# Kernel optimization log

Hardware: AMD Instinct MI355X
Metric: run time of the kernel (lower is better)

The kernel has to match this reference:

```python
import jax, jax.numpy as jnp
from jax import lax
import numpy as np

DECAY = 0.9
THRESH = 1.0


def setup_inputs() -> dict:
    key = jax.random.key(0)
    k1, k2, k3 = jax.random.split(key, 3)
    B, T, I, H, O = 64, 256, 1024, 2048, 1024
    x = jax.random.normal(k1, (B, T, I), dtype=jnp.float32)
    W1 = jax.random.normal(k2, (I, H), dtype=jnp.float32) * (1.0 / np.sqrt(I))
    b1 = jnp.zeros((H,), dtype=jnp.float32)
    W2 = jax.random.normal(k3, (H, O), dtype=jnp.float32) * (1.0 / np.sqrt(H))
    b2 = jnp.zeros((O,), dtype=jnp.float32)
    return {"x": x, "W1": W1, "b1": b1, "W2": W2, "b2": b2}


def reference(x, W1, b1, W2, b2):
    B, T, I = x.shape
    H = W1.shape[1]
    # Batch fc1 across all timesteps in one GEMM: [B,T,H]
    cur = jnp.einsum('bti,ih->bth', x, W1) + b1
    cur_tm = jnp.swapaxes(cur, 0, 1)  # [T,B,H] time-major for scan

    def step(carry, cur_t):
        mem, _ = carry
        mem = mem * DECAY + cur_t * (1.0 - DECAY)
        fired = mem > THRESH
        spk = jnp.where(fired, 1.0, 0.0).astype(mem.dtype)
        mem = jnp.where(fired, 0.0, mem)
        return (mem, spk), None

    mem0 = jnp.zeros((B, H), dtype=x.dtype)
    spk0 = jnp.zeros((B, H), dtype=x.dtype)
    (_, spk_last), _ = lax.scan(step, (mem0, spk0), cur_tm)
    # fc2 applied only to the final spike pattern, as in the original
    return spk_last @ W2 + b2
```

## Files before the change

kernel.cpp:

```cpp
#include <hip/hip_runtime.h>


typedef __attribute__((ext_vector_type(16))) float f32x16;
typedef __attribute__((ext_vector_type(8))) short s16x8;

#define GPTR(p) ((const __attribute__((address_space(1))) void*)(p))
#define SPTR(p) ((__attribute__((address_space(3))) void*)(p))

static constexpr int Bsz = 64, Tsz = 256, Isz = 1024, Hsz = 2048, Osz = 1024;
static constexpr int BK = 32;
static constexpr int NKT = Isz / BK;
static constexpr int AH_OFF = 0, AL_OFF = 8192, BH_OFF = 16384, BL_OFF = 24576;
static constexpr int BUFEL = 32768;
static constexpr int SCAN_STRIDE = 260;
static constexpr int LDS_USHORTS = 128 * SCAN_STRIDE * 2;

__device__ __forceinline__ unsigned short f2bf(float f) {
  unsigned u = __float_as_uint(f);
  u += 0x7FFFu + ((u >> 16) & 1u);
  return (unsigned short)(u >> 16);
}
__device__ __forceinline__ float bf2f(unsigned short h) {
  return __uint_as_float(((unsigned)h) << 16);
}

__global__ void split_x_kernel(const float* __restrict__ x,
                               unsigned short* __restrict__ hi,
                               unsigned short* __restrict__ lo) {
  const long i = (long)blockIdx.x * 256 + threadIdx.x;
  const float4 v = ((const float4*)x)[i];
  const unsigned short hx = f2bf(v.x), hy = f2bf(v.y), hz = f2bf(v.z), hw = f2bf(v.w);
  ushort4 H, L;
  H.x = hx; H.y = hy; H.z = hz; H.w = hw;
  L.x = f2bf(v.x - bf2f(hx));
  L.y = f2bf(v.y - bf2f(hy));
  L.z = f2bf(v.z - bf2f(hz));
  L.w = f2bf(v.w - bf2f(hw));
  ((ushort4*)hi)[i] = H;
  ((ushort4*)lo)[i] = L;
}

__global__ void w1_transpose_split_kernel(const float* __restrict__ W1,
                                          unsigned short* __restrict__ wh,
                                          unsigned short* __restrict__ wl) {
  __shared__ float tile[32][33];
  const int h0 = blockIdx.x * 32;
  const int i0 = blockIdx.y * 32;
  const int c = threadIdx.x & 31;
  const int r4 = threadIdx.x >> 5;
#pragma unroll
  for (int s = 0; s < 4; ++s) {
    const int r = r4 + s * 8;
    tile[r][c] = W1[(long)(i0 + r) * Hsz + h0 + c];
  }
  __syncthreads();
#pragma unroll
  for (int s = 0; s < 4; ++s) {
    const int hr = r4 + s * 8;
    const float v = tile[c][hr];
    const unsigned short hh = f2bf(v);
    wh[(long)(h0 + hr) * Isz + i0 + c] = hh;
    wl[(long)(h0 + hr) * Isz + i0 + c] = f2bf(v - bf2f(hh));
  }
}

__global__ __launch_bounds__(512, 2) void gemm1_scan_kernel(
    const unsigned short* __restrict__ xh, const unsigned short* __restrict__ xl,
    const unsigned short* __restrict__ wth, const unsigned short* __restrict__ wtl,
    const float* __restrict__ b1, float* __restrict__ spk) {
  __shared__ __align__(16) unsigned short lds[LDS_USHORTS];

  const int tid = threadIdx.x;
  const int l = tid & 63;
  const int w = tid >> 6;
  const int wm = w >> 2;
  const int wn = w & 3;
  const int b = blockIdx.y;
  const int hb = blockIdx.x * 256;

  const int srow = tid >> 2;
  const int gch8 = ((tid & 3) ^ ((tid >> 3) & 3)) * 8;
  const long aoff0 = (long)(b * Tsz + srow) * Isz + gch8;
  const long aoff1 = (long)(b * Tsz + 128 + srow) * Isz + gch8;
  const long boff0 = (long)(hb + srow) * Isz + gch8;
  const long boff1 = (long)(hb + 128 + srow) * Isz + gch8;
  const unsigned short* gAh0 = xh + aoff0;  const unsigned short* gAh1 = xh + aoff1;
  const unsigned short* gAl0 = xl + aoff0;  const unsigned short* gAl1 = xl + aoff1;
  const unsigned short* gBh0 = wth + boff0; const unsigned short* gBh1 = wth + boff1;
  const unsigned short* gBl0 = wtl + boff0; const unsigned short* gBl1 = wtl + boff1;

#define STG(OFF, G0, G1, KT) do {                                                      \
    unsigned short* d_ = lds + ((KT) & 1) * BUFEL + (OFF) + tid * 8;                   \
    __builtin_amdgcn_global_load_lds(GPTR((G0) + (long)(KT) * BK), SPTR(d_), 16, 0, 0);\
    __builtin_amdgcn_global_load_lds(GPTR((G1) + (long)(KT) * BK), SPTR(d_ + 4096), 16, 0, 0); \
  } while (0)

  const int lr = l & 31;
  const int swzf = (l >> 1) & 3;
  const int chK0 = (((l >> 5)) ^ swzf) * 8;
  const int chK1 = ((2 + (l >> 5)) ^ swzf) * 8;
  const int abase = (wm * 128 + lr) * 32;
  const int bbase = (wn * 64 + lr) * 32;

  f32x16 acc[4][2];
#pragma unroll
  for (int i = 0; i < 4; ++i)
#pragma unroll
    for (int j = 0; j < 2; ++j) acc[i][j] = (f32x16)(0.f);

#define MM(MI, NI, AF, BF) \
  acc[MI][NI] = __builtin_amdgcn_mfma_f32_32x32x16_bf16(AF, BF, acc[MI][NI], 0, 0, 0)

#define BAR() __builtin_amdgcn_s_barrier()
#define LGKM0() do { asm volatile("s_waitcnt lgkmcnt(0)" ::: "memory");                \
    __builtin_amdgcn_sched_barrier(0); } while (0)

  STG(AH_OFF, gAh0, gAh1, 0);
  STG(BH_OFF, gBh0, gBh1, 0);
  STG(AL_OFF, gAl0, gAl1, 0);
  STG(BL_OFF, gBl0, gBl1, 0);
  asm volatile("s_waitcnt vmcnt(0)" ::: "memory");
  BAR();

  s16x8 Ah0[4], Ah1[4], Al0[4], Al1[4], Bh0[2], Bh1[2], Bl0[2], Bl1[2];

  for (int kt = 0; kt < NKT; ++kt) {
    const unsigned short* p = lds + (kt & 1) * BUFEL;
    const bool st = (kt + 1) < NKT;

#pragma unroll
    for (int mi = 0; mi < 4; ++mi) {
      Ah0[mi] = *(const s16x8*)(p + AH_OFF + abase + mi * 1024 + chK0);
      Ah1[mi] = *(const s16x8*)(p + AH_OFF + abase + mi * 1024 + chK1);
    }
#pragma unroll
    for (int ni = 0; ni < 2; ++ni) {
      Bh0[ni] = *(const s16x8*)(p + BH_OFF + bbase + ni * 1024 + chK0);
      Bh1[ni] = *(const s16x8*)(p + BH_OFF + bbase + ni * 1024 + chK1);
    }
    if (st) { STG(AH_OFF, gAh0, gAh1, kt + 1); STG(BH_OFF, gBh0, gBh1, kt + 1); }
    BAR();
    LGKM0();
    __builtin_amdgcn_s_setprio(1);
    MM(0, 0, Ah0[0], Bh0[0]); MM(0, 1, Ah0[0], Bh0[1]);
    MM(1, 0, Ah0[1], Bh0[0]); MM(1, 1, Ah0[1], Bh0[1]);
    MM(2, 0, Ah0[2], Bh0[0]); MM(2, 1, Ah0[2], Bh0[1]);
    MM(3, 0, Ah0[3], Bh0[0]); MM(3, 1, Ah0[3], Bh0[1]);
    MM(0, 0, Ah1[0], Bh1[0]); MM(0, 1, Ah1[0], Bh1[1]);
    MM(1, 0, Ah1[1], Bh1[0]); MM(1, 1, Ah1[1], Bh1[1]);
    MM(2, 0, Ah1[2], Bh1[0]); MM(2, 1, Ah1[2], Bh1[1]);
    MM(3, 0, Ah1[3], Bh1[0]); MM(3, 1, Ah1[3], Bh1[1]);
    __builtin_amdgcn_s_setprio(0);
    if (st) asm volatile("s_waitcnt vmcnt(4)" ::: "memory");
    else    asm volatile("s_waitcnt vmcnt(0)" ::: "memory");
    BAR();

#pragma unroll
    for (int mi = 0; mi < 4; ++mi) {
      Al0[mi] = *(const s16x8*)(p + AL_OFF + abase + mi * 1024 + chK0);
      Al1[mi] = *(const s16x8*)(p + AL_OFF + abase + mi * 1024 + chK1);
    }
#pragma unroll
    for (int ni = 0; ni < 2; ++ni) {
      Bl0[ni] = *(const s16x8*)(p + BL_OFF + bbase + ni * 1024 + chK0);
      Bl1[ni] = *(const s16x8*)(p + BL_OFF + bbase + ni * 1024 + chK1);
    }
    if (st) { STG(AL_OFF, gAl0, gAl1, kt + 1); STG(BL_OFF, gBl0, gBl1, kt + 1); }
    BAR();
    LGKM0();
    __builtin_amdgcn_s_setprio(1);
    MM(0, 0, Ah0[0], Bl0[0]); MM(0, 1, Ah0[0], Bl0[1]);
    MM(1, 0, Ah0[1], Bl0[0]); MM(1, 1, Ah0[1], Bl0[1]);
    MM(2, 0, Ah0[2], Bl0[0]); MM(2, 1, Ah0[2], Bl0[1]);
    MM(3, 0, Ah0[3], Bl0[0]); MM(3, 1, Ah0[3], Bl0[1]);
    MM(0, 0, Ah1[0], Bl1[0]); MM(0, 1, Ah1[0], Bl1[1]);
    MM(1, 0, Ah1[1], Bl1[0]); MM(1, 1, Ah1[1], Bl1[1]);
    MM(2, 0, Ah1[2], Bl1[0]); MM(2, 1, Ah1[2], Bl1[1]);
    MM(3, 0, Ah1[3], Bl1[0]); MM(3, 1, Ah1[3], Bl1[1]);
    MM(0, 0, Al0[0], Bh0[0]); MM(0, 1, Al0[0], Bh0[1]);
    MM(1, 0, Al0[1], Bh0[0]); MM(1, 1, Al0[1], Bh0[1]);
    MM(2, 0, Al0[2], Bh0[0]); MM(2, 1, Al0[2], Bh0[1]);
    MM(3, 0, Al0[3], Bh0[0]); MM(3, 1, Al0[3], Bh0[1]);
    MM(0, 0, Al1[0], Bh1[0]); MM(0, 1, Al1[0], Bh1[1]);
    MM(1, 0, Al1[1], Bh1[0]); MM(1, 1, Al1[1], Bh1[1]);
    MM(2, 0, Al1[2], Bh1[0]); MM(2, 1, Al1[2], Bh1[1]);
    MM(3, 0, Al1[3], Bh1[0]); MM(3, 1, Al1[3], Bh1[1]);
    __builtin_amdgcn_s_setprio(0);
    asm volatile("s_waitcnt vmcnt(4)" ::: "memory");
    BAR();
  }

  __syncthreads();
  float* scanbuf = reinterpret_cast<float*>(lds);
  float memv = 0.f;
  int fired = 0;
  const float b1v = b1[hb + ((tid < 256) ? tid : 0)];

  for (int rnd = 0; rnd < 2; ++rnd) {
    if (wm == rnd) {
#pragma unroll
      for (int mi = 0; mi < 4; ++mi)
#pragma unroll
        for (int ni = 0; ni < 2; ++ni) {
          const int col = wn * 64 + ni * 32 + lr;
#pragma unroll
          for (int r = 0; r < 16; ++r) {
            const int trow = mi * 32 + (r & 3) + 8 * (r >> 2) + 4 * (l >> 5);
            scanbuf[trow * SCAN_STRIDE + col] = acc[mi][ni][r];
          }
        }
    }
    __syncthreads();
    if (tid < 256) {
      for (int t = 0; t < 128; ++t) {
        const float c = scanbuf[t * SCAN_STRIDE + tid] + b1v;
        memv = memv * 0.9f + c * 0.1f;
        fired = memv > 1.0f;
        if (fired) memv = 0.f;
      }
    }
    __syncthreads();
  }
  if (tid < 256) spk[(long)b * Hsz + hb + tid] = fired ? 1.0f : 0.0f;
}

__global__ void gemm2_kernel(const float* __restrict__ spk, const float* __restrict__ W2,
                             const float* __restrict__ b2, float* __restrict__ out) {
  __shared__ int s_cnt[256];
  __shared__ int s_off[257];
  __shared__ int s_list[Hsz];
  const int b = blockIdx.x;
  const int tid = threadIdx.x;
  int hs[8];
  int c = 0;
#pragma unroll
  for (int e = 0; e < 8; ++e) {
    const int h = tid * 8 + e;
    if (spk[(long)b * Hsz + h] > 0.5f) hs[c++] = h;
  }
  s_cnt[tid] = c;
  __syncthreads();
  if (tid == 0) {
    int s = 0;
    for (int i = 0; i < 256; ++i) { s_off[i] = s; s += s_cnt[i]; }
    s_off[256] = s;
  }
  __syncthreads();
  {
    const int base = s_off[tid];
    for (int i = 0; i < c; ++i) s_list[base + i] = hs[i];
  }
  __syncthreads();
  const int total = s_off[256];
#pragma unroll
  for (int q = 0; q < 4; ++q) {
    const int o = q * 256 + tid;
    float v = b2[o];
    for (int i = 0; i < total; ++i) v += W2[(long)s_list[i] * Osz + o];
    out[(long)b * Osz + o] = v;
  }
}

extern "C" void kernel_launch(void* const* d_in, const int* in_sizes, int n_in,
                              void* d_out, int out_size, void* d_ws, size_t ws_size,
                              hipStream_t stream) {
  const float* x = (const float*)d_in[0];
  const float* W1 = (const float*)d_in[1];
  const float* b1 = (const float*)d_in[2];
  const float* W2 = (const float*)d_in[3];
  const float* b2 = (const float*)d_in[4];
  float* out = (float*)d_out;

  unsigned short* xh = (unsigned short*)d_ws;
  unsigned short* xl = xh + (long)Bsz * Tsz * Isz;
  unsigned short* wh = xl + (long)Bsz * Tsz * Isz;
  unsigned short* wl = wh + (long)Hsz * Isz;
  float* spk = (float*)(wl + (long)Hsz * Isz);

  split_x_kernel<<<(Bsz * Tsz * Isz) / (256 * 4), 256, 0, stream>>>(x, xh, xl);
  w1_transpose_split_kernel<<<dim3(Hsz / 32, Isz / 32), 256, 0, stream>>>(W1, wh, wl);
  gemm1_scan_kernel<<<dim3(8, 64), 512, 0, stream>>>(xh, xl, wh, wl, b1, spk);
  gemm2_kernel<<<Bsz, 256, 0, stream>>>(spk, W2, b2, out);
}
```

Measured before the change: 213.4 us.

## Use 4 waves per block with 128x128 warp tiles and split LDS waits

Halves the threads per GEMM block from 512 to 256, so each wave now computes a 128x128 output tile (4x4 MFMA accumulators) instead of 128x64. Each thread issues four global-to-LDS loads per stage instead of two. The fragment loads are split into two halves with partial lgkmcnt waits, so MFMAs on the first half can start while the second half is still loading. This aims to raise register-level operand reuse and cut LDS read traffic per MFMA. In exchange it uses many more accumulator registers per wave and has fewer waves to hide latency.

New measurement: 209.0 us. -2.1%, faster.

```diff
diff --git a/kernel.cpp b/kernel.cpp
--- a/kernel.cpp
+++ b/kernel.cpp
@@ -64,7 +64,7 @@
   }
 }
 
-__global__ __launch_bounds__(512, 2) void gemm1_scan_kernel(
+__global__ __launch_bounds__(256, 1) void gemm1_scan_kernel(
     const unsigned short* __restrict__ xh, const unsigned short* __restrict__ xl,
     const unsigned short* __restrict__ wth, const unsigned short* __restrict__ wtl,
     const float* __restrict__ b1, float* __restrict__ spk) {
@@ -73,26 +73,24 @@
   const int tid = threadIdx.x;
   const int l = tid & 63;
   const int w = tid >> 6;
-  const int wm = w >> 2;
-  const int wn = w & 3;
+  const int wm = w >> 1;
+  const int wn = w & 1;
   const int b = blockIdx.y;
   const int hb = blockIdx.x * 256;
 
   const int srow = tid >> 2;
   const int gch8 = ((tid & 3) ^ ((tid >> 3) & 3)) * 8;
-  const long aoff0 = (long)(b * Tsz + srow) * Isz + gch8;
-  const long aoff1 = (long)(b * Tsz + 128 + srow) * Isz + gch8;
-  const long boff0 = (long)(hb + srow) * Isz + gch8;
-  const long boff1 = (long)(hb + 128 + srow) * Isz + gch8;
-  const unsigned short* gAh0 = xh + aoff0;  const unsigned short* gAh1 = xh + aoff1;
-  const unsigned short* gAl0 = xl + aoff0;  const unsigned short* gAl1 = xl + aoff1;
-  const unsigned short* gBh0 = wth + boff0; const unsigned short* gBh1 = wth + boff1;
-  const unsigned short* gBl0 = wtl + boff0; const unsigned short* gBl1 = wtl + boff1;
-
-#define STG(OFF, G0, G1, KT) do {                                                      \
-    unsigned short* d_ = lds + ((KT) & 1) * BUFEL + (OFF) + tid * 8;                   \
-    __builtin_amdgcn_global_load_lds(GPTR((G0) + (long)(KT) * BK), SPTR(d_), 16, 0, 0);\
-    __builtin_amdgcn_global_load_lds(GPTR((G1) + (long)(KT) * BK), SPTR(d_ + 4096), 16, 0, 0); \
+  const unsigned short* gAh = xh + (long)(b * Tsz + srow) * Isz + gch8;
+  const unsigned short* gAl = xl + (long)(b * Tsz + srow) * Isz + gch8;
+  const unsigned short* gBh = wth + (long)(hb + srow) * Isz + gch8;
+  const unsigned short* gBl = wtl + (long)(hb + srow) * Isz + gch8;
+
+#define STG(OFF, G, KT) do {                                                              \
+    unsigned short* d_ = lds + ((KT) & 1) * BUFEL + (OFF) + tid * 8;                      \
+    __builtin_amdgcn_global_load_lds(GPTR((G) + (long)(KT) * BK), SPTR(d_), 16, 0, 0);    \
+    __builtin_amdgcn_global_load_lds(GPTR((G) + 64 * Isz + (long)(KT) * BK), SPTR(d_ + 2048), 16, 0, 0); \
+    __builtin_amdgcn_global_load_lds(GPTR((G) + 128 * Isz + (long)(KT) * BK), SPTR(d_ + 4096), 16, 0, 0); \
+    __builtin_amdgcn_global_load_lds(GPTR((G) + 192 * Isz + (long)(KT) * BK), SPTR(d_ + 6144), 16, 0, 0); \
   } while (0)
 
   const int lr = l & 31;
@@ -100,93 +98,93 @@
   const int chK0 = (((l >> 5)) ^ swzf) * 8;
   const int chK1 = ((2 + (l >> 5)) ^ swzf) * 8;
   const int abase = (wm * 128 + lr) * 32;
-  const int bbase = (wn * 64 + lr) * 32;
-
-  f32x16 acc[4][2];
+  const int bbase = (wn * 128 + lr) * 32;
+
+  f32x16 acc[4][4];
 #pragma unroll
   for (int i = 0; i < 4; ++i)
 #pragma unroll
-    for (int j = 0; j < 2; ++j) acc[i][j] = (f32x16)(0.f);
+    for (int j = 0; j < 4; ++j) acc[i][j] = (f32x16)(0.f);
 
 #define MM(MI, NI, AF, BF) \
   acc[MI][NI] = __builtin_amdgcn_mfma_f32_32x32x16_bf16(AF, BF, acc[MI][NI], 0, 0, 0)
 
 #define BAR() __builtin_amdgcn_s_barrier()
-#define LGKM0() do { asm volatile("s_waitcnt lgkmcnt(0)" ::: "memory");                \
-    __builtin_amdgcn_sched_barrier(0); } while (0)
-
-  STG(AH_OFF, gAh0, gAh1, 0);
-  STG(BH_OFF, gBh0, gBh1, 0);
-  STG(AL_OFF, gAl0, gAl1, 0);
-  STG(BL_OFF, gBl0, gBl1, 0);
-  asm volatile("s_waitcnt vmcnt(0)" ::: "memory");
+#define SBAR() __builtin_amdgcn_sched_barrier(0)
+#define WAITLGKM(N) do { asm volatile("s_waitcnt lgkmcnt(" #N ")" ::: "memory"); SBAR(); } while (0)
+
+  STG(AH_OFF, gAh, 0);
+  STG(BH_OFF, gBh, 0);
+  STG(AL_OFF, gAl, 0);
+  STG(BL_OFF, gBl, 0);
+  asm volatile("s_waitcnt vmcnt(8)" ::: "memory");
   BAR();
 
-  s16x8 Ah0[4], Ah1[4], Al0[4], Al1[4], Bh0[2], Bh1[2], Bl0[2], Bl1[2];
+  s16x8 Ah0[4], Ah1[4], Al0[4], Al1[4], Bh0[4], Bh1[4], Bl0[4], Bl1[4];
 
   for (int kt = 0; kt < NKT; ++kt) {
     const unsigned short* p = lds + (kt & 1) * BUFEL;
     const bool st = (kt + 1) < NKT;
 
 #pragma unroll
-    for (int mi = 0; mi < 4; ++mi) {
-      Ah0[mi] = *(const s16x8*)(p + AH_OFF + abase + mi * 1024 + chK0);
-      Ah1[mi] = *(const s16x8*)(p + AH_OFF + abase + mi * 1024 + chK1);
-    }
-#pragma unroll
-    for (int ni = 0; ni < 2; ++ni) {
-      Bh0[ni] = *(const s16x8*)(p + BH_OFF + bbase + ni * 1024 + chK0);
-      Bh1[ni] = *(const s16x8*)(p + BH_OFF + bbase + ni * 1024 + chK1);
-    }
-    if (st) { STG(AH_OFF, gAh0, gAh1, kt + 1); STG(BH_OFF, gBh0, gBh1, kt + 1); }
-    BAR();
-    LGKM0();
+    for (int mi = 0; mi < 4; ++mi) Ah0[mi] = *(const s16x8*)(p + AH_OFF + abase + mi * 1024 + chK0);
+#pragma unroll
+    for (int ni = 0; ni < 4; ++ni) Bh0[ni] = *(const s16x8*)(p + BH_OFF + bbase + ni * 1024 + chK0);
+    SBAR();
+#pragma unroll
+    for (int mi = 0; mi < 4; ++mi) Ah1[mi] = *(const s16x8*)(p + AH_OFF + abase + mi * 1024 + chK1);
+#pragma unroll
+    for (int ni = 0; ni < 4; ++ni) Bh1[ni] = *(const s16x8*)(p + BH_OFF + bbase + ni * 1024 + chK1);
+    if (st) { STG(AH_OFF, gAh, kt + 1); STG(BH_OFF, gBh, kt + 1); }
+    WAITLGKM(8);
     __builtin_amdgcn_s_setprio(1);
-    MM(0, 0, Ah0[0], Bh0[0]); MM(0, 1, Ah0[0], Bh0[1]);
-    MM(1, 0, Ah0[1], Bh0[0]); MM(1, 1, Ah0[1], Bh0[1]);
-    MM(2, 0, Ah0[2], Bh0[0]); MM(2, 1, Ah0[2], Bh0[1]);
-    MM(3, 0, Ah0[3], Bh0[0]); MM(3, 1, Ah0[3], Bh0[1]);
-    MM(0, 0, Ah1[0], Bh1[0]); MM(0, 1, Ah1[0], Bh1[1]);
-    MM(1, 0, Ah1[1], Bh1[0]); MM(1, 1, Ah1[1], Bh1[1]);
-    MM(2, 0, Ah1[2], Bh1[0]); MM(2, 1, Ah1[2], Bh1[1]);
-    MM(3, 0, Ah1[3], Bh1[0]); MM(3, 1, Ah1[3], Bh1[1]);
+#pragma unroll
+    for (int mi = 0; mi < 4; ++mi)
+#pragma unroll
+      for (int ni = 0; ni < 4; ++ni) MM(mi, ni, Ah0[mi], Bh0[ni]);
+    WAITLGKM(0);
+#pragma unroll
+    for (int mi = 0; mi < 4; ++mi)
+#pragma unroll
+      for (int ni = 0; ni < 4; ++ni) MM(mi, ni, Ah1[mi], Bh1[ni]);
     __builtin_amdgcn_s_setprio(0);
-    if (st) asm volatile("s_waitcnt vmcnt(4)" ::: "memory");
+    if (st) asm volatile("s_waitcnt vmcnt(8)" ::: "memory");
     else    asm volatile("s_waitcnt vmcnt(0)" ::: "memory");
     BAR();
 
+#pragma unroll
+    for (int ni = 0; ni < 4; ++ni) {
+      Bl0[ni] = *(const s16x8*)(p + BL_OFF + bbase + ni * 1024 + chK0);
+      Bl1[ni] = *(const s16x8*)(p + BL_OFF + bbase + ni * 1024 + chK1);
+    }
+    SBAR();
 #pragma unroll
     for (int mi = 0; mi < 4; ++mi) {
       Al0[mi] = *(const s16x8*)(p + AL_OFF + abase + mi * 1024 + chK0);
       Al1[mi] = *(const s16x8*)(p + AL_OFF + abase + mi * 1024 + chK1);
     }
-#pragma unroll
-    for (int ni = 0; ni < 2; ++ni) {
-      Bl0[ni] = *(const s16x8*)(p + BL_OFF + bbase + ni * 1024 + chK0);
-      Bl1[ni] = *(const s16x8*)(p + BL_OFF + bbase + ni * 1024 + chK1);
-    }
-    if (st) { STG(AL_OFF, gAl0, gAl1, kt + 1); STG(BL_OFF, gBl0, gBl1, kt + 1); }
-    BAR();
-    LGKM0();
+    if (st) { STG(AL_OFF, gAl, kt + 1); STG(BL_OFF, gBl, kt + 1); }
+    WAITLGKM(8);
     __builtin_amdgcn_s_setprio(1);
-    MM(0, 0, Ah0[0], Bl0[0]); MM(0, 1, Ah0[0], Bl0[1]);
-    MM(1, 0, Ah0[1], Bl0[0]); MM(1, 1, Ah0[1], Bl0[1]);
-    MM(2, 0, Ah0[2], Bl0[0]); MM(2, 1, Ah0[2], Bl0[1]);
-    MM(3, 0, Ah0[3], Bl0[0]); MM(3, 1, Ah0[3], Bl0[1]);
-    MM(0, 0, Ah1[0], Bl1[0]); MM(0, 1, Ah1[0], Bl1[1]);
-    MM(1, 0, Ah1[1], Bl1[0]); MM(1, 1, Ah1[1], Bl1[1]);
-    MM(2, 0, Ah1[2], Bl1[0]); MM(2, 1, Ah1[2], Bl1[1]);
-    MM(3, 0, Ah1[3], Bl1[0]); MM(3, 1, Ah1[3], Bl1[1]);
-    MM(0, 0, Al0[0], Bh0[0]); MM(0, 1, Al0[0], Bh0[1]);
-    MM(1, 0, Al0[1], Bh0[0]); MM(1, 1, Al0[1], Bh0[1]);
-    MM(2, 0, Al0[2], Bh0[0]); MM(2, 1, Al0[2], Bh0[1]);
-    MM(3, 0, Al0[3], Bh0[0]); MM(3, 1, Al0[3], Bh0[1]);
-    MM(0, 0, Al1[0], Bh1[0]); MM(0, 1, Al1[0], Bh1[1]);
-    MM(1, 0, Al1[1], Bh1[0]); MM(1, 1, Al1[1], Bh1[1]);
-    MM(2, 0, Al1[2], Bh1[0]); MM(2, 1, Al1[2], Bh1[1]);
-    MM(3, 0, Al1[3], Bh1[0]); MM(3, 1, Al1[3], Bh1[1]);
+#pragma unroll
+    for (int mi = 0; mi < 4; ++mi)
+#pragma unroll
+      for (int ni = 0; ni < 4; ++ni) MM(mi, ni, Ah0[mi], Bl0[ni]);
+#pragma unroll
+    for (int mi = 0; mi < 4; ++mi)
+#pragma unroll
+      for (int ni = 0; ni < 4; ++ni) MM(mi, ni, Ah1[mi], Bl1[ni]);
+    WAITLGKM(0);
+#pragma unroll
+    for (int mi = 0; mi < 4; ++mi)
+#pragma unroll
+      for (int ni = 0; ni < 4; ++ni) MM(mi, ni, Al0[mi], Bh0[ni]);
+#pragma unroll
+    for (int mi = 0; mi < 4; ++mi)
+#pragma unroll
+      for (int ni = 0; ni < 4; ++ni) MM(mi, ni, Al1[mi], Bh1[ni]);
     __builtin_amdgcn_s_setprio(0);
-    asm volatile("s_waitcnt vmcnt(4)" ::: "memory");
+    asm volatile("s_waitcnt vmcnt(8)" ::: "memory");
     BAR();
   }
 
@@ -194,15 +192,15 @@
   float* scanbuf = reinterpret_cast<float*>(lds);
   float memv = 0.f;
   int fired = 0;
-  const float b1v = b1[hb + ((tid < 256) ? tid : 0)];
+  const float b1v = b1[hb + tid];
 
   for (int rnd = 0; rnd < 2; ++rnd) {
     if (wm == rnd) {
 #pragma unroll
       for (int mi = 0; mi < 4; ++mi)
 #pragma unroll
-        for (int ni = 0; ni < 2; ++ni) {
-          const int col = wn * 64 + ni * 32 + lr;
+        for (int ni = 0; ni < 4; ++ni) {
+          const int col = wn * 128 + ni * 32 + lr;
 #pragma unroll
           for (int r = 0; r < 16; ++r) {
             const int trow = mi * 32 + (r & 3) + 8 * (r >> 2) + 4 * (l >> 5);
@@ -211,7 +209,7 @@
         }
     }
     __syncthreads();
-    if (tid < 256) {
+    {
       for (int t = 0; t < 128; ++t) {
         const float c = scanbuf[t * SCAN_STRIDE + tid] + b1v;
         memv = memv * 0.9f + c * 0.1f;
@@ -221,7 +219,7 @@
     }
     __syncthreads();
   }
-  if (tid < 256) spk[(long)b * Hsz + hb + tid] = fired ? 1.0f : 0.0f;
+  spk[(long)b * Hsz + hb + tid] = fired ? 1.0f : 0.0f;
 }
 
 __global__ void gemm2_kernel(const float* __restrict__ spk, const float* __restrict__ W2,
@@ -279,6 +277,6 @@
 
   split_x_kernel<<<(Bsz * Tsz * Isz) / (256 * 4), 256, 0, stream>>>(x, xh, xl);
   w1_transpose_split_kernel<<<dim3(Hsz / 32, Isz / 32), 256, 0, stream>>>(W1, wh, wl);
-  gemm1_scan_kernel<<<dim3(8, 64), 512, 0, stream>>>(xh, xl, wh, wl, b1, spk);
+  gemm1_scan_kernel<<<dim3(8, 64), 256, 0, stream>>>(xh, xl, wh, wl, b1, spk);
   gemm2_kernel<<<Bsz, 256, 0, stream>>>(spk, W2, b2, out);
 }
```
